# Optimization experiments

Measured on AMD Instinct MI355X. Metric: run time of the kernel, lower is better.

Reference implementation:

```python
import jax, jax.numpy as jnp
import numpy as np

N = 6144      # total nodes = num_data_qubits + num_checks
NQ = 3072     # num_data_qubits
D = 128       # hidden_dim
H = 4         # attention heads
C = D // H    # per-head channels (GATConv out_channels)
F_IN = 10     # node_feature_dim
L = 4         # num_gnn_layers
E = 393216    # num edges (before self-loops)


def _ln(x, g, b):
    m = x.mean(-1, keepdims=True)
    v = ((x - m) ** 2).mean(-1, keepdims=True)
    return (x - m) / jnp.sqrt(v + 1e-5) * g + b


def setup_inputs() -> dict:
    key = jax.random.key(0)
    ks = iter(jax.random.split(key, 64))

    def nrm(shape, scale):
        return jax.random.normal(next(ks), shape, jnp.float32) * scale

    inp = {}
    inp["node_features"] = nrm((N, F_IN), 1.0)
    inp["edge_index"] = jax.random.randint(next(ks), (2, E), 0, N, jnp.int32)
    inp["partner_encoding"] = nrm((N, D), 1.0)
    # node embedding MLP
    inp["emb_W"] = nrm((F_IN, D), F_IN ** -0.5)
    inp["emb_b"] = jnp.zeros((D,), jnp.float32)
    inp["emb_ln_g"] = jnp.ones((D,), jnp.float32)
    inp["emb_ln_b"] = jnp.zeros((D,), jnp.float32)
    # GAT layers (stacked over L)
    inp["gat_W"] = nrm((L, D, D), D ** -0.5)
    inp["gat_a_src"] = nrm((L, H, C), C ** -0.5)
    inp["gat_a_dst"] = nrm((L, H, C), C ** -0.5)
    inp["gat_b"] = jnp.zeros((L, D), jnp.float32)
    inp["ln_g"] = jnp.ones((L, D), jnp.float32)
    inp["ln_b"] = jnp.zeros((L, D), jnp.float32)
    # cross-panel multihead attention
    for nm in ["Wq", "Wk", "Wv", "Wo"]:
        inp[nm] = nrm((D, D), D ** -0.5)
    for nm in ["bq", "bk", "bv", "bo"]:
        inp[nm] = jnp.zeros((D,), jnp.float32)
    inp["ca_ln_g"] = jnp.ones((D,), jnp.float32)
    inp["ca_ln_b"] = jnp.zeros((D,), jnp.float32)
    # policy head
    inp["pW1"] = nrm((D, D), D ** -0.5); inp["pb1"] = jnp.zeros((D,), jnp.float32)
    inp["pW2"] = nrm((D, D // 2), D ** -0.5); inp["pb2"] = jnp.zeros((D // 2,), jnp.float32)
    inp["pW3"] = nrm((D // 2, 2), (D // 2) ** -0.5); inp["pb3"] = jnp.zeros((2,), jnp.float32)
    # value head
    inp["vW1"] = nrm((D, D), D ** -0.5); inp["vb1"] = jnp.zeros((D,), jnp.float32)
    inp["vW2"] = nrm((D, D // 2), D ** -0.5); inp["vb2"] = jnp.zeros((D // 2,), jnp.float32)
    inp["vW3"] = nrm((D // 2, 1), (D // 2) ** -0.5); inp["vb3"] = jnp.zeros((1,), jnp.float32)
    return inp


def reference(node_features, edge_index, partner_encoding,
              emb_W, emb_b, emb_ln_g, emb_ln_b,
              gat_W, gat_a_src, gat_a_dst, gat_b, ln_g, ln_b,
              Wq, bq, Wk, bk, Wv, bv, Wo, bo, ca_ln_g, ca_ln_b,
              pW1, pb1, pW2, pb2, pW3, pb3,
              vW1, vb1, vW2, vb2, vW3, vb3):
    # PyG GATConv default: add self-loops
    loops = jnp.arange(N, dtype=edge_index.dtype)
    src = jnp.concatenate([edge_index[0], loops])  # message source j
    dst = jnp.concatenate([edge_index[1], loops])  # aggregation target i

    x = jax.nn.relu(_ln(node_features @ emb_W + emb_b, emb_ln_g, emb_ln_b))

    for l in range(L):
        h = (x @ gat_W[l]).reshape(N, H, C)
        a_s = (h * gat_a_src[l]).sum(-1)  # [N,H]
        a_d = (h * gat_a_dst[l]).sum(-1)  # [N,H]
        e = jax.nn.leaky_relu(a_s[src] + a_d[dst], 0.2)  # [E+N,H]
        # segment softmax over edges sharing destination node
        mx = jax.ops.segment_max(e, dst, num_segments=N)
        ex = jnp.exp(e - mx[dst])
        denom = jax.ops.segment_sum(ex, dst, num_segments=N)
        alpha = ex / (denom[dst] + 1e-16)
        out = jax.ops.segment_sum(alpha[:, :, None] * h[src], dst, num_segments=N)
        out = out.reshape(N, D) + gat_b[l]
        x = _ln(x + jax.nn.relu(out), ln_g[l], ln_b[l])

    # cross-panel multihead attention (eval mode, batch of 1)
    q = (x @ Wq + bq).reshape(N, H, C)
    k = (partner_encoding @ Wk + bk).reshape(N, H, C)
    v = (partner_encoding @ Wv + bv).reshape(N, H, C)
    att = jax.nn.softmax(jnp.einsum('nhd,mhd->hnm', q, k) / np.float32(np.sqrt(C)), axis=-1)
    xa = jnp.einsum('hnm,mhd->nhd', att, v).reshape(N, D) @ Wo + bo
    x = _ln(x + xa, ca_ln_g, ca_ln_b)

    dq = x[:NQ]
    logits = jax.nn.relu(jax.nn.relu(dq @ pW1 + pb1) @ pW2 + pb2) @ pW3 + pb3
    pooled = x.mean(0, keepdims=True)
    value = jax.nn.relu(jax.nn.relu(pooled @ vW1 + vb1) @ vW2 + vb2) @ vW3 + vb3
    return logits, value, x
```

## Files before the change

### kernel.cpp

```cpp
#include <hip/hip_runtime.h>
#include <hip/hip_bf16.h>

#define N_NODES 6144
#define NQ_ 3072
#define D 128
#define H 4
#define C 32
#define F_IN 10
#define L_LAYERS 4
#define E_EDGES 393216
#define E_TOT (E_EDGES + N_NODES)
#define SPLITS 8
#define KV_PER (N_NODES / SPLITS)
#define NT_TOT (N_NODES / 32)
#define LOG2E 1.4426950408889634f

typedef __attribute__((ext_vector_type(8))) short bf16x8;
typedef __attribute__((ext_vector_type(4))) float f32x4;
typedef __attribute__((ext_vector_type(16))) float f32x16;

__device__ __forceinline__ unsigned short f2bf(float f) {
  unsigned u = __float_as_uint(f);
  unsigned r = (u + 0x7fffu + ((u >> 16) & 1u)) >> 16;
  return (unsigned short)r;
}

__device__ __forceinline__ float bf2f(unsigned short s) {
  return __uint_as_float(((unsigned)s) << 16);
}

__device__ __forceinline__ unsigned cvtpk(float lo, float hi) {
  unsigned r;
  asm volatile("v_cvt_pk_bf16_f32 %0, %1, %2" : "=v"(r) : "v"(lo), "v"(hi));
  return r;
}

#define P32SWAP(a, b) asm volatile("v_permlane32_swap_b32 %0, %1" : "+v"(a), "+v"(b))

#define MFMA32(A, B, CIN) __builtin_amdgcn_mfma_f32_32x32x16_bf16(A, B, CIN, 0, 0, 0)

__device__ __forceinline__ float red128_sum(float v, float* tmp2, int tid) {
#pragma unroll
  for (int m = 1; m < 64; m <<= 1) v += __shfl_xor(v, m, 64);
  __syncthreads();
  if ((tid & 63) == 0) tmp2[tid >> 6] = v;
  __syncthreads();
  return tmp2[0] + tmp2[1];
}

__device__ __forceinline__ void red128_sum2(float& a, float& b, float* tmp4, int tid) {
#pragma unroll
  for (int m = 1; m < 64; m <<= 1) {
    a += __shfl_xor(a, m, 64);
    b += __shfl_xor(b, m, 64);
  }
  __syncthreads();
  if ((tid & 63) == 0) {
    tmp4[(tid >> 6) * 2]     = a;
    tmp4[(tid >> 6) * 2 + 1] = b;
  }
  __syncthreads();
  a = tmp4[0] + tmp4[2];
  b = tmp4[1] + tmp4[3];
}

__device__ __forceinline__ f32x16 tile_gemm128(const unsigned short* __restrict__ A,
                                               const unsigned short* __restrict__ Bt,
                                               int row0, int col0, int qc, int hi) {
  const unsigned short* ap = A + (size_t)(row0 + qc) * 128 + hi * 8;
  const unsigned short* bp = Bt + (size_t)(col0 + qc) * 128 + hi * 8;
  f32x16 o = {0.f};
#pragma unroll
  for (int kk = 0; kk < 8; kk++) {
    bf16x8 a = *(const bf16x8*)(ap + kk * 16);
    bf16x8 b = *(const bf16x8*)(bp + kk * 16);
    o = MFMA32(a, b, o);
  }
  return o;
}

__global__ void k_zero(int* cnt, int* cur, float* pooled) {
  int i = blockIdx.x * blockDim.x + threadIdx.x;
  if (i < N_NODES) { cnt[i] = 0; cur[i] = 0; }
  if (i < D) pooled[i] = 0.f;
}

__global__ void k_hist(const int* __restrict__ dst, int* __restrict__ cnt) {
  for (int i = blockIdx.x * blockDim.x + threadIdx.x; i < E_EDGES; i += gridDim.x * blockDim.x)
    atomicAdd(&cnt[dst[i]], 1);
}

__global__ void k_scan(const int* __restrict__ cnt, int* __restrict__ indptr) {
  __shared__ int ps[256];
  int tid = threadIdx.x;
  const int CH = N_NODES / 256;
  int base = tid * CH;
  int loc[CH];
  int s = 0;
#pragma unroll
  for (int i = 0; i < CH; i++) { loc[i] = cnt[base + i] + 1; s += loc[i]; }
  ps[tid] = s;
  __syncthreads();
  for (int off = 1; off < 256; off <<= 1) {
    int v = (tid >= off) ? ps[tid - off] : 0;
    __syncthreads();
    ps[tid] += v;
    __syncthreads();
  }
  int run = (tid == 0) ? 0 : ps[tid - 1];
#pragma unroll
  for (int i = 0; i < CH; i++) { indptr[base + i] = run; run += loc[i]; }
  if (tid == 255) indptr[N_NODES] = run;
}

__global__ void k_scatter(const int* __restrict__ src, const int* __restrict__ dst,
                          const int* __restrict__ indptr, int* __restrict__ cur,
                          int* __restrict__ sorted) {
  for (int i = blockIdx.x * blockDim.x + threadIdx.x; i < E_TOT; i += gridDim.x * blockDim.x) {
    if (i < E_EDGES) {
      int d = dst[i];
      int p = atomicAdd(&cur[d], 1);
      sorted[indptr[d] + p] = src[i];
    } else {
      int n = i - E_EDGES;
      int p = atomicAdd(&cur[n], 1);
      sorted[indptr[n] + p] = n;
    }
  }
}

__global__ __launch_bounds__(128) void k_embed(const float* __restrict__ nf,
                                               const float* __restrict__ W,
                                               const float* __restrict__ b,
                                               const float* __restrict__ g,
                                               const float* __restrict__ bb,
                                               float* __restrict__ x,
                                               unsigned short* __restrict__ xbf) {
  int n = blockIdx.x, j = threadIdx.x;
  __shared__ float f[F_IN];
  __shared__ float tmp4[4];
  if (j < F_IN) f[j] = nf[n * F_IN + j];
  __syncthreads();
  float acc = b[j];
#pragma unroll
  for (int k = 0; k < F_IN; k++) acc += f[k] * W[k * D + j];
  float s1 = acc, s2 = acc * acc;
  red128_sum2(s1, s2, tmp4, j);
  float mean = s1 * (1.f / D);
  float var = s2 * (1.f / D) - mean * mean;
  float y = (acc - mean) * rsqrtf(var + 1e-5f) * g[j] + bb[j];
  y = fmaxf(y, 0.f);
  x[n * D + j] = y;
  xbf[n * D + j] = f2bf(y);
}

__global__ void k_wprep(const float* __restrict__ W, unsigned short* __restrict__ wt) {
  int i = blockIdx.x * 256 + threadIdx.x;
  int l = i >> 14, rem = i & 16383, j = rem >> 7, k = rem & 127;
  wt[i] = f2bf(W[l * 16384 + k * 128 + j]);
}

__global__ void k_wqkvprep(const float* __restrict__ Wq, const float* __restrict__ Wk,
                           const float* __restrict__ Wv, const float* __restrict__ W1,
                           const float* __restrict__ W2, const float* __restrict__ Wo,
                           unsigned short* __restrict__ wqt, unsigned short* __restrict__ wkt,
                           unsigned short* __restrict__ wvt, unsigned short* __restrict__ w1t,
                           unsigned short* __restrict__ w2t, unsigned short* __restrict__ wot) {
  int i = blockIdx.x * 256 + threadIdx.x;
  if (i < 65536) {
    int m = i >> 14, loc = i & 16383, j = loc >> 7, k = loc & 127;
    const float* src = (m == 0) ? Wq : (m == 1) ? Wk : (m == 2) ? Wv : W1;
    unsigned short* dst = (m == 0) ? wqt : (m == 1) ? wkt : (m == 2) ? wvt : w1t;
    dst[loc] = f2bf(src[k * 128 + j]);
  } else if (i < 73728) {
    int loc = i - 65536, j = loc >> 7, k = loc & 127;
    w2t[loc] = f2bf(W2[k * 64 + j]);
  } else if (i < 90112) {
    int loc = i - 73728, j = loc >> 7, k = loc & 127;
    wot[loc] = f2bf(Wo[k * 128 + j]);
  }
}

__global__ void k_pebf(const float* __restrict__ pe, unsigned short* __restrict__ pebf) {
  int i = blockIdx.x * 256 + threadIdx.x;
  float4 v = *(const float4*)(pe + (size_t)i * 4);
  unsigned lo = (unsigned)f2bf(v.x) | ((unsigned)f2bf(v.y) << 16);
  unsigned hi = (unsigned)f2bf(v.z) | ((unsigned)f2bf(v.w) << 16);
  *(uint2*)(pebf + (size_t)i * 4) = make_uint2(lo, hi);
}

__global__ __launch_bounds__(256) void k_gat_gemm(const unsigned short* __restrict__ xbf,
                                                  const unsigned short* __restrict__ wt,
                                                  unsigned short* __restrict__ hbf) {
  int t = threadIdx.x;
  int w = t >> 6, l = t & 63, qc = l & 31, hi = l >> 5;
  int tile = blockIdx.x * 4 + w;
  int row0 = (tile >> 2) * 32, col0 = (tile & 3) * 32;
  f32x16 o = tile_gemm128(xbf, wt, row0, col0, qc, hi);
#pragma unroll
  for (int r = 0; r < 16; r++) {
    int rr = (r & 3) + 8 * (r >> 2) + 4 * hi;
    hbf[(size_t)(row0 + rr) * D + col0 + qc] = f2bf(o[r]);
  }
}

__global__ __launch_bounds__(128) void k_gat_attn(const unsigned short* __restrict__ hbf,
                                                  const float* __restrict__ asrc,
                                                  const float* __restrict__ adst,
                                                  float* __restrict__ a_s,
                                                  float* __restrict__ a_d) {
  int t = threadIdx.x;
  int ni = t >> 4, j = t & 15;
  int n = blockIdx.x * 8 + ni;
  const unsigned short* hp = hbf + (size_t)n * D + j * 8;
  float p = 0.f, q = 0.f;
#pragma unroll
  for (int c = 0; c < 8; c++) {
    float hv = bf2f(hp[c]);
    p += hv * asrc[j * 8 + c];
    q += hv * adst[j * 8 + c];
  }
  p += __shfl_xor(p, 1); p += __shfl_xor(p, 2);
  q += __shfl_xor(q, 1); q += __shfl_xor(q, 2);
  if ((j & 3) == 0) {
    int head = j >> 2;
    a_s[n * H + head] = p * LOG2E;
    a_d[n * H + head] = q * LOG2E;
  }
}

__device__ __forceinline__ float leaky(float v) { return v > 0.f ? v : 0.2f * v; }

__global__ __launch_bounds__(256) void k_gat_agg(const unsigned short* __restrict__ hbf,
                                                 const float* __restrict__ a_s,
                                                 const float* __restrict__ a_d,
                                                 const int* __restrict__ indptr,
                                                 const int* __restrict__ sorted,
                                                 const float* __restrict__ gb,
                                                 const float* __restrict__ g,
                                                 const float* __restrict__ bb,
                                                 float* __restrict__ x,
                                                 unsigned short* __restrict__ xbf) {
  int n = blockIdx.x, tid = threadIdx.x;
  int wv = tid >> 6, l = tid & 63;
  int beg = indptr[n], end = indptr[n + 1];
  __shared__ int s_src[256];
  __shared__ float s_ex[256 * 4];
  __shared__ float2 red2[4][64];
  __shared__ float rtmp[16];
  __shared__ float tmp8[8];
  float4 ad = *(const float4*)&a_d[n * H];
  int hsel = l >> 4;
  float accx = 0.f, accy = 0.f;
  float d0 = 0.f, d1 = 0.f, d2 = 0.f, d3 = 0.f;

  for (int c0 = beg; c0 < end; c0 += 256) {
    __syncthreads();
    int e = c0 + tid;
    if (e < end) {
      int s = sorted[e];
      s_src[tid] = s;
      float4 as = *(const float4*)&a_s[s * H];
      float e0 = exp2f(leaky(as.x + ad.x));
      float e1 = exp2f(leaky(as.y + ad.y));
      float e2 = exp2f(leaky(as.z + ad.z));
      float e3 = exp2f(leaky(as.w + ad.w));
      s_ex[tid * 4 + 0] = e0;
      s_ex[tid * 4 + 1] = e1;
      s_ex[tid * 4 + 2] = e2;
      s_ex[tid * 4 + 3] = e3;
      d0 += e0; d1 += e1; d2 += e2; d3 += e3;
    }
    __syncthreads();
    int nc = min(256, end - c0);
#pragma unroll 4
    for (int i = wv; i < nc; i += 4) {
      float al = s_ex[i * 4 + hsel];
      int s = s_src[i];
      unsigned dw = *(const unsigned*)(hbf + (size_t)s * D + l * 2);
      accx += al * bf2f((unsigned short)(dw & 0xffff));
      accy += al * bf2f((unsigned short)(dw >> 16));
    }
  }
  red2[wv][l] = make_float2(accx, accy);
#pragma unroll
  for (int m = 1; m < 64; m <<= 1) {
    d0 += __shfl_xor(d0, m, 64);
    d1 += __shfl_xor(d1, m, 64);
    d2 += __shfl_xor(d2, m, 64);
    d3 += __shfl_xor(d3, m, 64);
  }
  if (l == 0) {
    rtmp[wv * 4 + 0] = d0; rtmp[wv * 4 + 1] = d1;
    rtmp[wv * 4 + 2] = d2; rtmp[wv * 4 + 3] = d3;
  }
  __syncthreads();

  float y = 0.f;
  int c = tid;
  if (tid < 128) {
    const float* rp0 = (const float*)&red2[0][c >> 1];
    const float* rp1 = (const float*)&red2[1][c >> 1];
    const float* rp2 = (const float*)&red2[2][c >> 1];
    const float* rp3 = (const float*)&red2[3][c >> 1];
    int par = c & 1;
    float sum = rp0[par] + rp1[par] + rp2[par] + rp3[par];
    int hd = c >> 5;
    float dd = rtmp[hd] + rtmp[4 + hd] + rtmp[8 + hd] + rtmp[12 + hd];
    float outv = sum * (1.f / (dd + 1e-16f)) + gb[c];
    y = x[n * D + c] + fmaxf(outv, 0.f);
  }
  float sy = y, syy = y * y;
#pragma unroll
  for (int m = 1; m < 64; m <<= 1) {
    sy += __shfl_xor(sy, m, 64);
    syy += __shfl_xor(syy, m, 64);
  }
  if (l == 0) { tmp8[wv * 2] = sy; tmp8[wv * 2 + 1] = syy; }
  __syncthreads();
  if (tid < 128) {
    float s1 = tmp8[0] + tmp8[2] + tmp8[4] + tmp8[6];
    float s2 = tmp8[1] + tmp8[3] + tmp8[5] + tmp8[7];
    float mean = s1 * (1.f / D);
    float var = s2 * (1.f / D) - mean * mean;
    float o = (y - mean) * rsqrtf(var + 1e-5f) * g[c] + bb[c];
    x[n * D + c] = o;
    xbf[n * D + c] = f2bf(o);
  }
}

__global__ __launch_bounds__(256) void k_qkv_mfma(const unsigned short* __restrict__ xbf,
                                                  const unsigned short* __restrict__ pebf,
                                                  const unsigned short* __restrict__ wqt,
                                                  const unsigned short* __restrict__ wkt,
                                                  const unsigned short* __restrict__ wvt,
                                                  const float* __restrict__ bq,
                                                  const float* __restrict__ bk,
                                                  const float* __restrict__ bv,
                                                  unsigned short* __restrict__ qbf,
                                                  unsigned short* __restrict__ kpk,
                                                  unsigned short* __restrict__ vpk) {
  int t = threadIdx.x;
  int w = t >> 6, l = t & 63, qc = l & 31, hi = l >> 5;
  int m = blockIdx.y;
  int row0 = blockIdx.x * 32, col0 = w * 32;
  const unsigned short* A = (m == 0) ? xbf : pebf;
  const unsigned short* Bt = (m == 0) ? wqt : (m == 1) ? wkt : wvt;
  f32x16 o = tile_gemm128(A, Bt, row0, col0, qc, hi);
  int c = col0 + qc;
  int hh = col0 >> 5;
  int kt = row0 >> 5;
  if (m == 0) {
    const float sc = 0.25503491f;
    float bias = bq[c];
#pragma unroll
    for (int r = 0; r < 16; r++) {
      int rr = (r & 3) + 8 * (r >> 2) + 4 * hi;
      qbf[(size_t)(row0 + rr) * D + c] = f2bf((o[r] + bias) * sc);
    }
  } else if (m == 1) {
    float bias = bk[c];
    int kfrag = (qc >> 4) & 1, khi = (qc >> 3) & 1, kj = qc & 7;
    unsigned short* base = kpk + ((((size_t)hh * NT_TOT + kt) * 2 + kfrag) * 64 + khi * 32) * 8 + kj;
#pragma unroll
    for (int r = 0; r < 16; r++) {
      int rr = (r & 3) + 8 * (r >> 2) + 4 * hi;
      base[rr * 8] = f2bf(o[r] + bias);
    }
  } else {
    float bias = bv[c];
#pragma unroll
    for (int r = 0; r < 16; r++) {
      int rr = (r & 3) + 8 * (r >> 2) + 4 * hi;
      int vfrag = (rr >> 4) & 1, vhi = (rr >> 3) & 1, vj = rr & 7;
      vpk[((((size_t)hh * NT_TOT + kt) * 2 + vfrag) * 64 + vhi * 32 + qc) * 8 + vj] =
          f2bf(o[r] + bias);
    }
  }
}

#define ALOAD(KA0, KA1, VB0_, VB1_, TI) do { \
  const unsigned short* kp_ = kB + (size_t)(TI) * 1024 + l8; \
  const unsigned short* vp_ = vB + (size_t)(TI) * 1024 + l8; \
  KA0 = *(const bf16x8*)(kp_); \
  KA1 = *(const bf16x8*)(kp_ + 512); \
  VB0_ = *(const bf16x8*)(vp_); \
  VB1_ = *(const bf16x8*)(vp_ + 512); \
} while (0)

#define TILE32(KA0, KA1, VB0_, VB1_, O, LS) do { \
  f32x16 s = MFMA32(KA0, qa0, zz16); \
  s = MFMA32(KA1, qa1, s); \
  float p0 = __builtin_amdgcn_exp2f(s[0]), p1 = __builtin_amdgcn_exp2f(s[1]); \
  float p2 = __builtin_amdgcn_exp2f(s[2]), p3 = __builtin_amdgcn_exp2f(s[3]); \
  float p4 = __builtin_amdgcn_exp2f(s[4]), p5 = __builtin_amdgcn_exp2f(s[5]); \
  float p6 = __builtin_amdgcn_exp2f(s[6]), p7 = __builtin_amdgcn_exp2f(s[7]); \
  float p8 = __builtin_amdgcn_exp2f(s[8]), p9 = __builtin_amdgcn_exp2f(s[9]); \
  float pa = __builtin_amdgcn_exp2f(s[10]), pc = __builtin_amdgcn_exp2f(s[11]); \
  float pd = __builtin_amdgcn_exp2f(s[12]), pe_ = __builtin_amdgcn_exp2f(s[13]); \
  float pf = __builtin_amdgcn_exp2f(s[14]), pg = __builtin_amdgcn_exp2f(s[15]); \
  LS += (((p0 + p1) + (p2 + p3)) + ((p4 + p5) + (p6 + p7))) + \
        (((p8 + p9) + (pa + pc)) + ((pd + pe_) + (pf + pg))); \
  unsigned x0_ = cvtpk(p0, p1), x1_ = cvtpk(p2, p3); \
  unsigned y0_ = cvtpk(p4, p5), y1_ = cvtpk(p6, p7); \
  P32SWAP(x0_, y0_); P32SWAP(x1_, y1_); \
  unsigned x2_ = cvtpk(p8, p9), x3_ = cvtpk(pa, pc); \
  unsigned y2_ = cvtpk(pd, pe_), y3_ = cvtpk(pf, pg); \
  P32SWAP(x2_, y2_); P32SWAP(x3_, y3_); \
  union { unsigned u[4]; bf16x8 v; } fa_, fb_; \
  fa_.u[0] = x0_; fa_.u[1] = x1_; fa_.u[2] = y0_; fa_.u[3] = y1_; \
  fb_.u[0] = x2_; fb_.u[1] = x3_; fb_.u[2] = y2_; fb_.u[3] = y3_; \
  O = MFMA32(VB0_, fa_.v, O); \
  O = MFMA32(VB1_, fb_.v, O); \
} while (0)

__global__ __launch_bounds__(256) void k_attn_split(const unsigned short* __restrict__ qbf,
                                                    const unsigned short* __restrict__ kpk,
                                                    const unsigned short* __restrict__ vpk,
                                                    unsigned short* __restrict__ po,
                                                    float* __restrict__ pl) {
  int hh = blockIdx.y;
  int sp = blockIdx.z;
  int t = threadIdx.x;
  int wid = t >> 6, l = t & 63;
  int qc = l & 31, hi = l >> 5;
  int l8 = l * 8;
  int q0w = blockIdx.x * 128 + wid * 32;

  const f32x16 zz16 = {0.f};

  const unsigned short* qp = qbf + (size_t)(q0w + qc) * D + hh * 32 + hi * 8;
  bf16x8 qa0 = *(const bf16x8*)(qp);
  bf16x8 qa1 = *(const bf16x8*)(qp + 16);

  const unsigned short* kB = kpk + ((size_t)hh * NT_TOT + sp * (KV_PER / 32)) * 1024;
  const unsigned short* vB = vpk + ((size_t)hh * NT_TOT + sp * (KV_PER / 32)) * 1024;

  f32x16 oA = {0.f}, oB = {0.f};
  float lsA = 0.f, lsB = 0.f;

  bf16x8 ka0, ka1, va0, va1, kb0r, kb1r, vb0r, vb1r;
  ALOAD(ka0, ka1, va0, va1, 0);
  const int NT = KV_PER / 32;
  for (int it = 0; it < NT; it += 2) {
    ALOAD(kb0r, kb1r, vb0r, vb1r, it + 1);
    TILE32(ka0, ka1, va0, va1, oA, lsA);
    if (it + 2 < NT) ALOAD(ka0, ka1, va0, va1, it + 2);
    TILE32(kb0r, kb1r, vb0r, vb1r, oB, lsB);
  }

  f32x16 o = oA + oB;
  float lsum = lsA + lsB;
  float lt = lsum + __shfl_xor(lsum, 32, 64);
  size_t pbase = (size_t)(sp * H + hh) * N_NODES + q0w + qc;
  unsigned short* pop = po + pbase * 32 + 4 * hi;
  uint2 v0, v1, v2, v3;
  v0.x = cvtpk(o[0], o[1]);   v0.y = cvtpk(o[2], o[3]);
  v1.x = cvtpk(o[4], o[5]);   v1.y = cvtpk(o[6], o[7]);
  v2.x = cvtpk(o[8], o[9]);   v2.y = cvtpk(o[10], o[11]);
  v3.x = cvtpk(o[12], o[13]); v3.y = cvtpk(o[14], o[15]);
  *(uint2*)(pop)      = v0;
  *(uint2*)(pop + 8)  = v1;
  *(uint2*)(pop + 16) = v2;
  *(uint2*)(pop + 24) = v3;
  if (l < 32) {
    pl[pbase] = lt;
  }
}

__global__ __launch_bounds__(256) void k_attn_combine(const unsigned short* __restrict__ po,
                                                      const float* __restrict__ pl,
                                                      unsigned short* __restrict__ xabf) {
  int t = blockIdx.x * 256 + threadIdx.x;
  int q = t >> 6, cp = t & 63;
  int c2 = cp * 2, hh = c2 >> 5, c = c2 & 31;
  int base = hh * N_NODES + q;
  const int SN = H * N_NODES;
  float ll = 0.f, olo = 0.f, ohi = 0.f;
#pragma unroll
  for (int s = 0; s < SPLITS; s++) {
    ll += pl[s * SN + base];
    unsigned dw = *(const unsigned*)(po + ((size_t)(s * SN + base)) * 32 + c);
    olo += bf2f((unsigned short)(dw & 0xffff));
    ohi += bf2f((unsigned short)(dw >> 16));
  }
  float inv = 1.f / ll;
  *(unsigned*)(xabf + (size_t)q * D + c2) = cvtpk(olo * inv, ohi * inv);
}

__global__ __launch_bounds__(256) void k_ca_gemm(const unsigned short* __restrict__ xabf,
                                                 const unsigned short* __restrict__ wot,
                                                 const float* __restrict__ bo,
                                                 float* __restrict__ yb) {
  int t = threadIdx.x;
  int w = t >> 6, l = t & 63, qc = l & 31, hi = l >> 5;
  int row0 = blockIdx.x * 32, col0 = w * 32;
  f32x16 o = tile_gemm128(xabf, wot, row0, col0, qc, hi);
  float bias = bo[col0 + qc];
#pragma unroll
  for (int r = 0; r < 16; r++) {
    int rr = (r & 3) + 8 * (r >> 2) + 4 * hi;
    yb[(size_t)(row0 + rr) * D + col0 + qc] = o[r] + bias;
  }
}

__global__ __launch_bounds__(128) void k_ca_ln(const float* __restrict__ yb,
                                               const float* __restrict__ g,
                                               const float* __restrict__ bb,
                                               float* __restrict__ x,
                                               unsigned short* __restrict__ xbf,
                                               float* __restrict__ pooled,
                                               float* __restrict__ outx) {
  int tid = threadIdx.x, r0 = blockIdx.x * 8;
  __shared__ float tmp4[4];
  float gv = g[tid], bv = bb[tid];
  float psum = 0.f;
#pragma unroll
  for (int r = 0; r < 8; r++) {
    int n = r0 + r;
    float y = x[n * D + tid] + yb[n * D + tid];
    float s1 = y, s2 = y * y;
    red128_sum2(s1, s2, tmp4, tid);
    float mean = s1 * (1.f / D);
    float var = s2 * (1.f / D) - mean * mean;
    float o = (y - mean) * rsqrtf(var + 1e-5f) * gv + bv;
    x[n * D + tid] = o;
    xbf[n * D + tid] = f2bf(o);
    outx[n * D + tid] = o;
    psum += o;
  }
  atomicAdd(&pooled[tid], psum);
}

__global__ __launch_bounds__(256) void k_policy1(const unsigned short* __restrict__ xbf,
                                                 const unsigned short* __restrict__ w1t,
                                                 const float* __restrict__ b1,
                                                 unsigned short* __restrict__ h1) {
  int t = threadIdx.x;
  int w = t >> 6, l = t & 63, qc = l & 31, hi = l >> 5;
  int row0 = blockIdx.x * 32, col0 = w * 32;
  f32x16 o = tile_gemm128(xbf, w1t, row0, col0, qc, hi);
  float bias = b1[col0 + qc];
#pragma unroll
  for (int r = 0; r < 16; r++) {
    int rr = (r & 3) + 8 * (r >> 2) + 4 * hi;
    h1[(size_t)(row0 + rr) * D + col0 + qc] = f2bf(fmaxf(o[r] + bias, 0.f));
  }
}

__global__ __launch_bounds__(128) void k_policy2(const unsigned short* __restrict__ h1,
                                                 const unsigned short* __restrict__ w2t,
                                                 const float* __restrict__ b2,
                                                 unsigned short* __restrict__ h2) {
  int t = threadIdx.x;
  int w = t >> 6, l = t & 63, qc = l & 31, hi = l >> 5;
  int row0 = blockIdx.x * 32, col0 = w * 32;
  f32x16 o = tile_gemm128(h1, w2t, row0, col0, qc, hi);
  float bias = b2[col0 + qc];
#pragma unroll
  for (int r = 0; r < 16; r++) {
    int rr = (r & 3) + 8 * (r >> 2) + 4 * hi;
    h2[(size_t)(row0 + rr) * 64 + col0 + qc] = f2bf(fmaxf(o[r] + bias, 0.f));
  }
}

__global__ __launch_bounds__(256) void k_policy3(const unsigned short* __restrict__ h2,
                                                 const float* __restrict__ W3,
                                                 const float* __restrict__ b3,
                                                 float* __restrict__ logits) {
  int t = threadIdx.x;
  int wv = t >> 6, l = t & 63;
  int n = blockIdx.x * 4 + wv;
  float h = bf2f(h2[(size_t)n * 64 + l]);
  float p0 = h * W3[l * 2];
  float p1 = h * W3[l * 2 + 1];
#pragma unroll
  for (int m = 1; m < 64; m <<= 1) { p0 += __shfl_xor(p0, m, 64); p1 += __shfl_xor(p1, m, 64); }
  if (l == 0) {
    logits[n * 2] = p0 + b3[0];
    logits[n * 2 + 1] = p1 + b3[1];
  }
}

__global__ __launch_bounds__(128) void k_value(const float* __restrict__ pooled,
                                               const float* __restrict__ W1,
                                               const float* __restrict__ b1,
                                               const float* __restrict__ W2,
                                               const float* __restrict__ b2,
                                               const float* __restrict__ W3,
                                               const float* __restrict__ b3,
                                               float* __restrict__ val) {
  int tid = threadIdx.x;
  __shared__ float ps[D], v1[D], v2[64];
  ps[tid] = pooled[tid] * (1.f / N_NODES);
  __syncthreads();
  float a = b1[tid];
  for (int kk = 0; kk < D; kk++) a += ps[kk] * W1[kk * D + tid];
  v1[tid] = fmaxf(a, 0.f);
  __syncthreads();
  if (tid < 64) {
    float a2 = b2[tid];
    for (int kk = 0; kk < D; kk++) a2 += v1[kk] * W2[kk * 64 + tid];
    v2[tid] = fmaxf(a2, 0.f);
  }
  __syncthreads();
  float p = (tid < 64) ? v2[tid] * W3[tid] : 0.f;
#pragma unroll
  for (int m = 1; m < 64; m <<= 1) p += __shfl_xor(p, m, 64);
  if (tid == 0) val[0] = p + b3[0];
}

extern "C" void kernel_launch(void* const* d_in, const int* in_sizes, int n_in,
                              void* d_out, int out_size, void* d_ws, size_t ws_size,
                              hipStream_t stream) {
  const float* nf   = (const float*)d_in[0];
  const int*   ei   = (const int*)d_in[1];
  const float* pe   = (const float*)d_in[2];
  const float* embW = (const float*)d_in[3];
  const float* embB = (const float*)d_in[4];
  const float* elng = (const float*)d_in[5];
  const float* elnb = (const float*)d_in[6];
  const float* gatW = (const float*)d_in[7];
  const float* aS   = (const float*)d_in[8];
  const float* aD   = (const float*)d_in[9];
  const float* gatB = (const float*)d_in[10];
  const float* lng  = (const float*)d_in[11];
  const float* lnb  = (const float*)d_in[12];
  const float* Wq   = (const float*)d_in[13];
  const float* Wk   = (const float*)d_in[14];
  const float* Wv   = (const float*)d_in[15];
  const float* Wo   = (const float*)d_in[16];
  const float* bq   = (const float*)d_in[17];
  const float* bk   = (const float*)d_in[18];
  const float* bv   = (const float*)d_in[19];
  const float* bo   = (const float*)d_in[20];
  const float* cag  = (const float*)d_in[21];
  const float* cab  = (const float*)d_in[22];
  const float* pW1  = (const float*)d_in[23];
  const float* pb1  = (const float*)d_in[24];
  const float* pW2  = (const float*)d_in[25];
  const float* pb2  = (const float*)d_in[26];
  const float* pW3  = (const float*)d_in[27];
  const float* pb3  = (const float*)d_in[28];
  const float* vW1  = (const float*)d_in[29];
  const float* vb1  = (const float*)d_in[30];
  const float* vW2  = (const float*)d_in[31];
  const float* vb2  = (const float*)d_in[32];
  const float* vW3  = (const float*)d_in[33];
  const float* vb3  = (const float*)d_in[34];

  float* fw = (float*)d_ws;
  float* x      = fw; fw += N_NODES * D;
  float* hbuf   = fw; fw += N_NODES * D;
  float* a_s    = fw; fw += N_NODES * H;
  float* a_d    = fw; fw += N_NODES * H;
  float* pooled = fw; fw += 128;
  float* pl     = fw; fw += SPLITS * H * N_NODES;
  unsigned short* ub = (unsigned short*)fw;
  unsigned short* po   = ub; ub += (size_t)SPLITS * H * N_NODES * 32;
  unsigned short* qbf  = ub; ub += N_NODES * D;
  unsigned short* kpk  = ub; ub += N_NODES * D;
  unsigned short* vpk  = ub; ub += N_NODES * D;
  unsigned short* xbf  = ub; ub += N_NODES * D;
  unsigned short* pebf = ub; ub += N_NODES * D;
  unsigned short* wtb  = ub; ub += L_LAYERS * D * D;
  unsigned short* wqt  = ub; ub += D * D;
  unsigned short* wkt  = ub; ub += D * D;
  unsigned short* wvt  = ub; ub += D * D;
  unsigned short* w1t  = ub; ub += D * D;
  unsigned short* w2t  = ub; ub += 64 * D;
  unsigned short* wot  = ub; ub += D * D;
  int* ib     = (int*)ub;
  int* cnt    = ib; ib += N_NODES;
  int* cur    = ib; ib += N_NODES;
  int* indptr = ib; ib += N_NODES + 16;
  int* sorted = ib;

  unsigned short* hbf  = (unsigned short*)hbuf;
  float* yb            = hbuf;
  unsigned short* xabf = kpk;
  unsigned short* h1   = qbf;
  unsigned short* h2   = qbf + (size_t)NQ_ * D;

  float* out    = (float*)d_out;
  float* logits = out;
  float* val    = out + NQ_ * 2;
  float* outx   = out + NQ_ * 2 + 1;

  const int* esrc = ei;
  const int* edst = ei + E_EDGES;

  hipLaunchKernelGGL(k_zero, dim3(24), dim3(256), 0, stream, cnt, cur, pooled);
  hipLaunchKernelGGL(k_hist, dim3(512), dim3(256), 0, stream, edst, cnt);
  hipLaunchKernelGGL(k_scan, dim3(1), dim3(256), 0, stream, cnt, indptr);
  hipLaunchKernelGGL(k_scatter, dim3(512), dim3(256), 0, stream, esrc, edst, indptr, cur, sorted);
  hipLaunchKernelGGL(k_embed, dim3(N_NODES), dim3(128), 0, stream, nf, embW, embB, elng, elnb, x, xbf);
  hipLaunchKernelGGL(k_wprep, dim3(L_LAYERS * D * D / 256), dim3(256), 0, stream, gatW, wtb);
  hipLaunchKernelGGL(k_wqkvprep, dim3(352), dim3(256), 0, stream,
                     Wq, Wk, Wv, pW1, pW2, Wo, wqt, wkt, wvt, w1t, w2t, wot);
  hipLaunchKernelGGL(k_pebf, dim3(N_NODES * D / 1024), dim3(256), 0, stream, pe, pebf);
  for (int l = 0; l < L_LAYERS; l++) {
    hipLaunchKernelGGL(k_gat_gemm, dim3(N_NODES / 32), dim3(256), 0, stream,
                       xbf, wtb + l * D * D, hbf);
    hipLaunchKernelGGL(k_gat_attn, dim3(N_NODES / 8), dim3(128), 0, stream,
                       hbf, aS + l * D, aD + l * D, a_s, a_d);
    hipLaunchKernelGGL(k_gat_agg, dim3(N_NODES), dim3(256), 0, stream,
                       hbf, a_s, a_d, indptr, sorted, gatB + l * D, lng + l * D, lnb + l * D, x, xbf);
  }
  hipLaunchKernelGGL(k_qkv_mfma, dim3(N_NODES / 32, 3), dim3(256), 0, stream,
                     xbf, pebf, wqt, wkt, wvt, bq, bk, bv, qbf, kpk, vpk);
  hipLaunchKernelGGL(k_attn_split, dim3(N_NODES / 128, H, SPLITS), dim3(256), 0, stream,
                     qbf, kpk, vpk, po, pl);
  hipLaunchKernelGGL(k_attn_combine, dim3(N_NODES * D / 512), dim3(256), 0, stream,
                     po, pl, xabf);
  hipLaunchKernelGGL(k_ca_gemm, dim3(N_NODES / 32), dim3(256), 0, stream, xabf, wot, bo, yb);
  hipLaunchKernelGGL(k_ca_ln, dim3(N_NODES / 8), dim3(128), 0, stream,
                     yb, cag, cab, x, xbf, pooled, outx);
  hipLaunchKernelGGL(k_policy1, dim3(NQ_ / 32), dim3(256), 0, stream, xbf, w1t, pb1, h1);
  hipLaunchKernelGGL(k_policy2, dim3(NQ_ / 32), dim3(128), 0, stream, h1, w2t, pb2, h2);
  hipLaunchKernelGGL(k_policy3, dim3(NQ_ / 4), dim3(256), 0, stream, h2, pW3, pb3, logits);
  hipLaunchKernelGGL(k_value, dim3(1), dim3(128), 0, stream,
                     pooled, vW1, vb1, vW2, vb2, vW3, vb3, val);
}
```

Before: 268.7 us.

## Merge prep kernels, vectorize GAT attention loads, batch gather loads in aggregation

Combines the zeroing, weight transpose/convert and partner-encoding bf16 conversion kernels into one launch to cut launch overhead. Vectorizes the per-node attention-coefficient dot products with 16-byte loads. Restructures the edge aggregation inner loop to issue eight independent gather loads before the FMAs, exposing memory-level parallelism. The unrolled gather raises register use, which may reduce occupancy in the aggregation kernel.

```diff
diff --git a/kernel.cpp b/kernel.cpp
--- a/kernel.cpp
+++ b/kernel.cpp
@@ -39,15 +39,6 @@
 
 #define MFMA32(A, B, CIN) __builtin_amdgcn_mfma_f32_32x32x16_bf16(A, B, CIN, 0, 0, 0)
 
-__device__ __forceinline__ float red128_sum(float v, float* tmp2, int tid) {
-#pragma unroll
-  for (int m = 1; m < 64; m <<= 1) v += __shfl_xor(v, m, 64);
-  __syncthreads();
-  if ((tid & 63) == 0) tmp2[tid >> 6] = v;
-  __syncthreads();
-  return tmp2[0] + tmp2[1];
-}
-
 __device__ __forceinline__ void red128_sum2(float& a, float& b, float* tmp4, int tid) {
 #pragma unroll
   for (int m = 1; m < 64; m <<= 1) {
@@ -79,11 +70,52 @@
   return o;
 }
 
-__global__ void k_zero(int* cnt, int* cur, float* pooled) {
-  int i = blockIdx.x * blockDim.x + threadIdx.x;
-  if (i < N_NODES) { cnt[i] = 0; cur[i] = 0; }
-  if (i < D) pooled[i] = 0.f;
-}
+__global__ void k_prep(int* cnt, int* cur, float* pooled,
+                       const float* __restrict__ gatW, unsigned short* __restrict__ wt,
+                       const float* __restrict__ Wq, const float* __restrict__ Wk,
+                       const float* __restrict__ Wv, const float* __restrict__ W1,
+                       const float* __restrict__ W2, const float* __restrict__ Wo,
+                       unsigned short* __restrict__ wqt, unsigned short* __restrict__ wkt,
+                       unsigned short* __restrict__ wvt, unsigned short* __restrict__ w1t,
+                       unsigned short* __restrict__ w2t, unsigned short* __restrict__ wot,
+                       const float* __restrict__ pe, unsigned short* __restrict__ pebf) {
+  int i = blockIdx.x * 256 + threadIdx.x;
+  if (i < 6272) {
+    if (i < N_NODES) { cnt[i] = 0; cur[i] = 0; }
+    else pooled[i - N_NODES] = 0.f;
+    return;
+  }
+  i -= 6272;
+  if (i < 65536) {
+    int l = i >> 14, rem = i & 16383, j = rem >> 7, k = rem & 127;
+    wt[i] = f2bf(gatW[l * 16384 + k * 128 + j]);
+    return;
+  }
+  i -= 65536;
+  if (i < 90112) {
+    if (i < 65536) {
+      int m = i >> 14, loc = i & 16383, j = loc >> 7, k = loc & 127;
+      const float* src = (m == 0) ? Wq : (m == 1) ? Wk : (m == 2) ? Wv : W1;
+      unsigned short* dst = (m == 0) ? wqt : (m == 1) ? wkt : (m == 2) ? wvt : w1t;
+      dst[loc] = f2bf(src[k * 128 + j]);
+    } else if (i < 73728) {
+      int loc = i - 65536, j = loc >> 7, k = loc & 127;
+      w2t[loc] = f2bf(W2[k * 64 + j]);
+    } else {
+      int loc = i - 73728, j = loc >> 7, k = loc & 127;
+      wot[loc] = f2bf(Wo[k * 128 + j]);
+    }
+    return;
+  }
+  i -= 90112;
+  if (i < N_NODES * D / 4) {
+    float4 v = ((const float4*)pe)[i];
+    unsigned lo = (unsigned)f2bf(v.x) | ((unsigned)f2bf(v.y) << 16);
+    unsigned hi = (unsigned)f2bf(v.z) | ((unsigned)f2bf(v.w) << 16);
+    *(uint2*)(pebf + (size_t)i * 4) = make_uint2(lo, hi);
+  }
+}
+#define PREP_ITEMS (6272 + 65536 + 90112 + N_NODES * D / 4)
 
 __global__ void k_hist(const int* __restrict__ dst, int* __restrict__ cnt) {
   for (int i = blockIdx.x * blockDim.x + threadIdx.x; i < E_EDGES; i += gridDim.x * blockDim.x)
@@ -154,41 +186,6 @@
   xbf[n * D + j] = f2bf(y);
 }
 
-__global__ void k_wprep(const float* __restrict__ W, unsigned short* __restrict__ wt) {
-  int i = blockIdx.x * 256 + threadIdx.x;
-  int l = i >> 14, rem = i & 16383, j = rem >> 7, k = rem & 127;
-  wt[i] = f2bf(W[l * 16384 + k * 128 + j]);
-}
-
-__global__ void k_wqkvprep(const float* __restrict__ Wq, const float* __restrict__ Wk,
-                           const float* __restrict__ Wv, const float* __restrict__ W1,
-                           const float* __restrict__ W2, const float* __restrict__ Wo,
-                           unsigned short* __restrict__ wqt, unsigned short* __restrict__ wkt,
-                           unsigned short* __restrict__ wvt, unsigned short* __restrict__ w1t,
-                           unsigned short* __restrict__ w2t, unsigned short* __restrict__ wot) {
-  int i = blockIdx.x * 256 + threadIdx.x;
-  if (i < 65536) {
-    int m = i >> 14, loc = i & 16383, j = loc >> 7, k = loc & 127;
-    const float* src = (m == 0) ? Wq : (m == 1) ? Wk : (m == 2) ? Wv : W1;
-    unsigned short* dst = (m == 0) ? wqt : (m == 1) ? wkt : (m == 2) ? wvt : w1t;
-    dst[loc] = f2bf(src[k * 128 + j]);
-  } else if (i < 73728) {
-    int loc = i - 65536, j = loc >> 7, k = loc & 127;
-    w2t[loc] = f2bf(W2[k * 64 + j]);
-  } else if (i < 90112) {
-    int loc = i - 73728, j = loc >> 7, k = loc & 127;
-    wot[loc] = f2bf(Wo[k * 128 + j]);
-  }
-}
-
-__global__ void k_pebf(const float* __restrict__ pe, unsigned short* __restrict__ pebf) {
-  int i = blockIdx.x * 256 + threadIdx.x;
-  float4 v = *(const float4*)(pe + (size_t)i * 4);
-  unsigned lo = (unsigned)f2bf(v.x) | ((unsigned)f2bf(v.y) << 16);
-  unsigned hi = (unsigned)f2bf(v.z) | ((unsigned)f2bf(v.w) << 16);
-  *(uint2*)(pebf + (size_t)i * 4) = make_uint2(lo, hi);
-}
-
 __global__ __launch_bounds__(256) void k_gat_gemm(const unsigned short* __restrict__ xbf,
                                                   const unsigned short* __restrict__ wt,
                                                   unsigned short* __restrict__ hbf) {
@@ -212,14 +209,17 @@
   int t = threadIdx.x;
   int ni = t >> 4, j = t & 15;
   int n = blockIdx.x * 8 + ni;
-  const unsigned short* hp = hbf + (size_t)n * D + j * 8;
-  float p = 0.f, q = 0.f;
-#pragma unroll
-  for (int c = 0; c < 8; c++) {
-    float hv = bf2f(hp[c]);
-    p += hv * asrc[j * 8 + c];
-    q += hv * adst[j * 8 + c];
-  }
+  bf16x8 hv = *(const bf16x8*)(hbf + (size_t)n * D + j * 8);
+  float4 a0 = *(const float4*)(asrc + j * 8);
+  float4 a1 = *(const float4*)(asrc + j * 8 + 4);
+  float4 d0 = *(const float4*)(adst + j * 8);
+  float4 d1 = *(const float4*)(adst + j * 8 + 4);
+  float h0 = bf2f(hv[0]), h1 = bf2f(hv[1]), h2 = bf2f(hv[2]), h3 = bf2f(hv[3]);
+  float h4 = bf2f(hv[4]), h5 = bf2f(hv[5]), h6 = bf2f(hv[6]), h7 = bf2f(hv[7]);
+  float p = h0 * a0.x + h1 * a0.y + h2 * a0.z + h3 * a0.w +
+            h4 * a1.x + h5 * a1.y + h6 * a1.z + h7 * a1.w;
+  float q = h0 * d0.x + h1 * d0.y + h2 * d0.z + h3 * d0.w +
+            h4 * d1.x + h5 * d1.y + h6 * d1.z + h7 * d1.w;
   p += __shfl_xor(p, 1); p += __shfl_xor(p, 2);
   q += __shfl_xor(q, 1); q += __shfl_xor(q, 2);
   if ((j & 3) == 0) {
@@ -251,6 +251,7 @@
   __shared__ float tmp8[8];
   float4 ad = *(const float4*)&a_d[n * H];
   int hsel = l >> 4;
+  const unsigned short* hb = hbf + l * 2;
   float accx = 0.f, accy = 0.f;
   float d0 = 0.f, d1 = 0.f, d2 = 0.f, d3 = 0.f;
 
@@ -273,13 +274,31 @@
     }
     __syncthreads();
     int nc = min(256, end - c0);
-#pragma unroll 4
-    for (int i = wv; i < nc; i += 4) {
+    int i = wv;
+    for (; i + 28 < nc; i += 32) {
+      int ss[8];
+      float aa[8];
+#pragma unroll
+      for (int u = 0; u < 8; u++) {
+        int idx = i + u * 4;
+        ss[u] = s_src[idx];
+        aa[u] = s_ex[idx * 4 + hsel];
+      }
+      unsigned dw[8];
+#pragma unroll
+      for (int u = 0; u < 8; u++) dw[u] = *(const unsigned*)(hb + (size_t)ss[u] * D);
+#pragma unroll
+      for (int u = 0; u < 8; u++) {
+        accx = fmaf(aa[u], bf2f((unsigned short)(dw[u] & 0xffff)), accx);
+        accy = fmaf(aa[u], bf2f((unsigned short)(dw[u] >> 16)), accy);
+      }
+    }
+    for (; i < nc; i += 4) {
       float al = s_ex[i * 4 + hsel];
       int s = s_src[i];
-      unsigned dw = *(const unsigned*)(hbf + (size_t)s * D + l * 2);
-      accx += al * bf2f((unsigned short)(dw & 0xffff));
-      accy += al * bf2f((unsigned short)(dw >> 16));
+      unsigned dw = *(const unsigned*)(hb + (size_t)s * D);
+      accx = fmaf(al, bf2f((unsigned short)(dw & 0xffff)), accx);
+      accy = fmaf(al, bf2f((unsigned short)(dw >> 16)), accy);
     }
   }
   red2[wv][l] = make_float2(accx, accy);
@@ -690,15 +709,13 @@
   const int* esrc = ei;
   const int* edst = ei + E_EDGES;
 
-  hipLaunchKernelGGL(k_zero, dim3(24), dim3(256), 0, stream, cnt, cur, pooled);
+  hipLaunchKernelGGL(k_prep, dim3((PREP_ITEMS + 255) / 256), dim3(256), 0, stream,
+                     cnt, cur, pooled, gatW, wtb, Wq, Wk, Wv, pW1, pW2, Wo,
+                     wqt, wkt, wvt, w1t, w2t, wot, pe, pebf);
   hipLaunchKernelGGL(k_hist, dim3(512), dim3(256), 0, stream, edst, cnt);
   hipLaunchKernelGGL(k_scan, dim3(1), dim3(256), 0, stream, cnt, indptr);
   hipLaunchKernelGGL(k_scatter, dim3(512), dim3(256), 0, stream, esrc, edst, indptr, cur, sorted);
   hipLaunchKernelGGL(k_embed, dim3(N_NODES), dim3(128), 0, stream, nf, embW, embB, elng, elnb, x, xbf);
-  hipLaunchKernelGGL(k_wprep, dim3(L_LAYERS * D * D / 256), dim3(256), 0, stream, gatW, wtb);
-  hipLaunchKernelGGL(k_wqkvprep, dim3(352), dim3(256), 0, stream,
-                     Wq, Wk, Wv, pW1, pW2, Wo, wqt, wkt, wvt, w1t, w2t, wot);
-  hipLaunchKernelGGL(k_pebf, dim3(N_NODES * D / 1024), dim3(256), 0, stream, pe, pebf);
   for (int l = 0; l < L_LAYERS; l++) {
     hipLaunchKernelGGL(k_gat_gemm, dim3(N_NODES / 32), dim3(256), 0, stream,
                        xbf, wtb + l * D * D, hbf);
```

New measurement: 263.2 us. -2.0%, faster.
